# Kernel optimization log

Hardware: AMD Instinct MI355X
Metric: run time of the kernel (lower is better)

The kernel has to match this reference:

```python
import jax, jax.numpy as jnp
import numpy as np

B, S, D, H, E, K, DH = 4, 1024, 1024, 8, 4, 2, 128


def setup_inputs() -> dict:
    key = jax.random.key(0)
    ks = jax.random.split(key, 9)
    std = 1.0 / np.sqrt(D)
    f = lambda k, shape, s: jax.random.normal(k, shape, dtype=jnp.float32) * s
    return {
        'q_src': f(ks[0], (B, S, D), 1.0),
        'k_src': f(ks[1], (B, S, D), 1.0),
        'v_src': f(ks[2], (B, S, D), 1.0),
        'Wq': f(ks[3], (H * DH, D), std),
        'Wk': f(ks[4], (H * DH, D), std),
        'Wv': f(ks[5], (H * E, D, DH), std),
        'Wo': f(ks[6], (H * E, DH, D), 1.0 / np.sqrt(H * DH)),
        'sel_v': f(ks[7], (H * E, D), std),
        'sel_o': f(ks[8], (H * E, D), std),
    }


def _route(src, selw):
    # sigmoid-gated per-head top-k expert selection (get_sel), eval mode
    g = jax.nn.sigmoid((src @ selw.T).reshape(*src.shape[:-1], H, E))  # [B,S,H,E]
    val, idx = jax.lax.top_k(g, K)
    # dense per-expert mixture weights: zeros except top-k sigmoid gates
    return (jax.nn.one_hot(idx, E, dtype=g.dtype) * val[..., None]).sum(-2)  # [B,S,H,E]


def reference(q_src, k_src, v_src, Wq, Wk, Wv, Wo, sel_v, sel_o):
    scale = (1.0 / np.sqrt(DH)) ** 0.5  # scale.sqrt() applied to both q and k
    q = ((q_src @ Wq.T) * scale).reshape(B, S, H, DH).transpose(0, 2, 1, 3)  # [B,H,S,DH]
    k = ((k_src @ Wk.T) * scale).reshape(B, S, H, DH).transpose(0, 2, 1, 3)

    wv = _route(k_src, sel_v)  # [B,S,H,E] V-expert gates (from keys)
    wo = _route(q_src, sel_o)  # [B,S,H,E] O-expert gates (from queries)

    # cvmm V: per-token top-k mixture of expert V projections
    v_all = jnp.einsum('bsd,hedc->bshec', v_src, Wv.reshape(H, E, D, DH))
    v = jnp.einsum('bshec,bshe->bhsc', v_all, wv)  # [B,H,S,DH]

    att = jax.nn.softmax(jnp.einsum('bhqc,bhkc->bhqk', q, k), axis=-1)
    res = jnp.einsum('bhqk,bhkc->bqhc', att, v)  # [B,S,H,DH]

    # cvmm O: weight per-head outputs by gates, project and sum over heads/experts
    resw = res[..., None, :] * wo[..., None]  # [B,S,H,E,DH]
    out = jnp.einsum('bshec,hecd->bsd', resw, Wo.reshape(H, E, DH, D))
    return out
```

## Files before the change

kernel.cpp:

```cpp
#include <hip/hip_runtime.h>

#define DEV __device__ __forceinline__

typedef __attribute__((ext_vector_type(8))) short s8v;
typedef __attribute__((ext_vector_type(4))) short s4v;
typedef __attribute__((ext_vector_type(4))) float f4v;

DEV unsigned short f2b(float f){
    unsigned u = __float_as_uint(f);
    u = (u + 0x7FFFu + ((u >> 16) & 1u)) >> 16;
    return (unsigned short)u;
}
DEV float b2f(short s){ return __uint_as_float(((unsigned)(unsigned short)s) << 16); }

DEV unsigned cvtpk(float lo, float hi){
    unsigned r;
    asm("v_cvt_pk_bf16_f32 %0, %1, %2" : "=v"(r) : "v"(lo), "v"(hi));
    return r;
}
DEV float exp2v(float x){
    float r;
    asm("v_exp_f32 %0, %1" : "=v"(r) : "v"(x));
    return r;
}

DEV void gload16(const void* g, void* l){
    __builtin_amdgcn_global_load_lds(
        (const __attribute__((address_space(1))) unsigned*)g,
        (__attribute__((address_space(3))) unsigned*)l, 16, 0, 0);
}


DEV void stage2(const short* A, const short* B, int sA, int sB, int kA, int kB,
                short* la, short* lb, int w, int lane){
    int srow = lane >> 3;
    int swcol = ((lane & 7) ^ srow) << 3;
    #pragma unroll
    for(int it = 0; it < 4; it++){
        int seg = (w << 2) + it;
        int row = (seg << 3) + srow;
        gload16(&A[(size_t)row * sA + kA + swcol], &la[seg << 9]);
        gload16(&B[(size_t)row * sB + kB + swcol], &lb[seg << 9]);
    }
}

DEV void mfma_block(const short* la, const short* lb, int wm, int wn, int qr, int grp, f4v acc[4][4]){
    #pragma unroll
    for(int ks = 0; ks < 2; ks++){
        s8v af[4], bf[4];
        #pragma unroll
        for(int m = 0; m < 4; m++)
            af[m] = *(const s8v*)&la[(wm + m * 16 + qr) * 64 + ((((ks << 2) + grp) ^ (qr & 7)) << 3)];
        #pragma unroll
        for(int n = 0; n < 4; n++)
            bf[n] = *(const s8v*)&lb[(wn + n * 16 + qr) * 64 + ((((ks << 2) + grp) ^ (qr & 7)) << 3)];
        #pragma unroll
        for(int m = 0; m < 4; m++)
            #pragma unroll
            for(int n = 0; n < 4; n++)
                acc[m][n] = __builtin_amdgcn_mfma_f32_16x16x32_bf16(af[m], bf[n], acc[m][n], 0, 0, 0);
    }
}

__global__ __launch_bounds__(256) void k_cvt(const float* s0, const float* s1, const float* s2,
                                             const float* s3, const float* s4,
                                             short* o0, short* o1, short* o2, short* o3, short* o4){
    int y = blockIdx.y;
    const float* s = (y == 0) ? s0 : (y == 1) ? s1 : (y == 2) ? s2 : (y == 3) ? s3 : s4;
    short* o = (y == 0) ? o0 : (y == 1) ? o1 : (y == 2) ? o2 : (y == 3) ? o3 : o4;
    int n8 = (y < 3) ? 524288 : 131072;
    int idx = blockIdx.x * 256 + threadIdx.x;
    if(idx < n8){
        const float4* f = (const float4*)(s + (size_t)idx * 8);
        float4 a = f[0], b = f[1];
        s8v v;
        v[0] = f2b(a.x); v[1] = f2b(a.y); v[2] = f2b(a.z); v[3] = f2b(a.w);
        v[4] = f2b(b.x); v[5] = f2b(b.y); v[6] = f2b(b.z); v[7] = f2b(b.w);
        *(s8v*)(o + (size_t)idx * 8) = v;
    }
}

__global__ __launch_bounds__(256) void k_transpose(const float* in, short* out, int R, int C){
    in  += (size_t)blockIdx.z * R * C;
    out += (size_t)blockIdx.z * R * C;
    __shared__ float t[32][33];
    int c0 = blockIdx.x * 32, r0 = blockIdx.y * 32;
    int tx = threadIdx.x & 31, ty = threadIdx.x >> 5;
    #pragma unroll
    for(int p = 0; p < 4; p++){
        int r = p * 8 + ty;
        t[r][tx] = in[(size_t)(r0 + r) * C + c0 + tx];
    }
    __syncthreads();
    #pragma unroll
    for(int p = 0; p < 4; p++){
        int c = p * 8 + ty;
        out[(size_t)(c0 + c) * R + r0 + tx] = (short)f2b(t[tx][c]);
    }
}

__global__ __launch_bounds__(256) void k_rlogits(const float* qsrc, const float* ksrc,
                                                 const float* selv, const float* selo,
                                                 float* part){
    int which = blockIdx.y;
    const float* src = which ? qsrc : ksrc;
    const float* sel = which ? selo : selv;
    int tt = blockIdx.x >> 3, ks = blockIdx.x & 7;
    int tok0 = tt << 7;
    __shared__ float lsrc[128][36];
    __shared__ float lsel[32][36];
    int tid = threadIdx.x;
    int ts = tid & 31, es = tid >> 5;
    float acc[4][4];
    #pragma unroll
    for(int j = 0; j < 4; j++)
        #pragma unroll
        for(int i = 0; i < 4; i++) acc[j][i] = 0.f;

    #pragma unroll 1
    for(int c = 0; c < 4; c++){
        int k0 = (ks << 7) + (c << 5);
        {
            int row = tid >> 1, half = tid & 1;
            const float4* g = (const float4*)(src + (size_t)(tok0 + row) * 1024 + k0 + half * 16);
            #pragma unroll
            for(int qq = 0; qq < 4; qq++){
                int qw = half * 4 + qq;
                *(float4*)&lsrc[row][((qw + row) & 7) * 4] = g[qq];
            }
        }
        {
            int row = tid >> 3, qw = tid & 7;
            *(float4*)&lsel[row][((qw + row) & 7) * 4] =
                *(const float4*)(sel + (size_t)row * 1024 + k0 + qw * 4);
        }
        __syncthreads();
        #pragma unroll
        for(int q = 0; q < 8; q++){
            float4 sv[4];
            #pragma unroll
            for(int i = 0; i < 4; i++){
                int e = es * 4 + i;
                sv[i] = *(const float4*)&lsel[e][((q + e) & 7) * 4];
            }
            int slot = ((q + ts) & 7) * 4;
            #pragma unroll
            for(int j = 0; j < 4; j++){
                float4 xv = *(const float4*)&lsrc[ts + 32 * j][slot];
                #pragma unroll
                for(int i = 0; i < 4; i++){
                    acc[j][i] = fmaf(xv.x, sv[i].x, acc[j][i]);
                    acc[j][i] = fmaf(xv.y, sv[i].y, acc[j][i]);
                    acc[j][i] = fmaf(xv.z, sv[i].z, acc[j][i]);
                    acc[j][i] = fmaf(xv.w, sv[i].w, acc[j][i]);
                }
            }
        }
        __syncthreads();
    }
    #pragma unroll
    for(int j = 0; j < 4; j++){
        int token = tok0 + ts + 32 * j;
        f4v st;
        #pragma unroll
        for(int i = 0; i < 4; i++) st[i] = acc[j][i];
        *(f4v*)&part[(((size_t)(ks * 2 + which) * 4096) + token) * 32 + es * 4] = st;
    }
}

__global__ __launch_bounds__(256) void k_rfinal(const float* part, float* wvp, float* wop){
    int which = blockIdx.y;
    float* wout = which ? wop : wvp;
    int tid = threadIdx.x;
    int tok = blockIdx.x * 32 + (tid >> 3), h = tid & 7;
    f4v sum = {0.f, 0.f, 0.f, 0.f};
    #pragma unroll
    for(int s = 0; s < 8; s++)
        sum += *(const f4v*)&part[(((size_t)(s * 2 + which) * 4096) + tok) * 32 + h * 4];
    float g[4];
    #pragma unroll
    for(int e = 0; e < 4; e++) g[e] = 1.0f / (1.0f + expf(-sum[e]));
    f4v out;
    #pragma unroll
    for(int e = 0; e < 4; e++){
        int rank = 0;
        #pragma unroll
        for(int j = 0; j < 4; j++)
            rank += (g[j] > g[e]) || (g[j] == g[e] && j < e);
        out[e] = (rank < 2) ? g[e] : 0.0f;
    }
    *(f4v*)&wout[(size_t)tok * 32 + h * 4] = out;
}

__global__ __launch_bounds__(256) void k_count(const float* wv, int* cntv){
    int he = blockIdx.x, tid = threadIdx.x;
    __shared__ int red[256];
    int c = 0;
    #pragma unroll
    for(int p = 0; p < 16; p++)
        c += (wv[(size_t)(p * 256 + tid) * 32 + he] > 0.f) ? 1 : 0;
    red[tid] = c;
    __syncthreads();
    for(int s = 128; s > 0; s >>= 1){
        if(tid < s) red[tid] += red[tid + s];
        __syncthreads();
    }
    if(tid == 0) cntv[he] = red[0];
}

__global__ __launch_bounds__(256) void k_scan(const int* cntv, int* basev, int* descv){
    __shared__ int ntl[33];
    int tid = threadIdx.x;
    if(tid == 0){
        int run = 0;
        for(int he = 0; he < 32; he++){
            ntl[he] = run;
            run += (cntv[he] + 127) >> 7;
        }
        ntl[32] = run;
    }
    __syncthreads();
    if(tid < 32) basev[tid] = ntl[tid] << 7;
    for(int i = tid; i < 544; i += 256){
        int d = -1;
        for(int he = 0; he < 32; he++)
            if(i >= ntl[he] && i < ntl[he + 1]) d = he;
        descv[i] = d;
    }
}

__global__ __launch_bounds__(256) void k_gather(const float* wv, const int* basev,
                                                int* idxv, float* gbufv, int* rpos){
    int he = blockIdx.x, h = he >> 2, e = he & 3;
    int tid = threadIdx.x, lane = tid & 63, w = tid >> 6;
    int base = basev[he];
    __shared__ int wsum[4];
    __shared__ int running;
    if(tid == 0) running = 0;
    __syncthreads();
    #pragma unroll 1
    for(int p = 0; p < 16; p++){
        int t = p * 256 + tid;
        float g = wv[(size_t)t * 32 + he];
        bool sel = g > 0.f;
        unsigned long long m = __ballot(sel);
        int lpref = __popcll(m & ((1ull << lane) - 1ull));
        if(lane == 0) wsum[w] = __popcll(m);
        __syncthreads();
        int rb = running;
        int woff = 0;
        #pragma unroll
        for(int j = 0; j < 4; j++) woff += (j < w) ? wsum[j] : 0;
        if(sel){
            int pos = base + rb + woff + lpref;
            idxv[pos] = t;
            gbufv[pos] = g;
            int slot = 0;
            #pragma unroll
            for(int j = 0; j < 4; j++)
                slot += (j < e && wv[(size_t)t * 32 + h * 4 + j] > 0.f) ? 1 : 0;
            rpos[(size_t)t * 16 + h * 2 + slot] = pos;
        }
        __syncthreads();
        if(tid == 0) running += wsum[0] + wsum[1] + wsum[2] + wsum[3];
        __syncthreads();
    }
    int tot = running;
    int aligned = (tot + 127) & ~127;
    for(int i = tid; i < aligned - tot; i += 256){
        idxv[base + tot + i] = 0;
        gbufv[base + tot + i] = 0.f;
    }
}

__global__ __launch_bounds__(256) void k_gemmg(const short* vsb, const short* wvt,
                                               const int* descv, const int* idxv,
                                               const float* gbufv, short* Cg){
    int he = descv[blockIdx.x];
    if(he < 0) return;
    int row0 = (int)blockIdx.x << 7;
    __shared__ __align__(16) short la[2][8192];
    __shared__ __align__(16) short lb[2][8192];
    __shared__ int lidx[128];
    int tid = threadIdx.x, lane = tid & 63, w = tid >> 6;
    if(tid < 128) lidx[tid] = idxv[row0 + tid];
    __syncthreads();
    int srow = lane >> 3;
    int swcol = ((lane & 7) ^ srow) << 3;
    int arow[4];
    #pragma unroll
    for(int it = 0; it < 4; it++) arow[it] = lidx[(((w << 2) + it) << 3) + srow];
    const short* Bb = wvt + ((size_t)he << 17);
    int wm = (w >> 1) << 6, wn = (w & 1) << 6;
    int qr = lane & 15, grp = lane >> 4;
    f4v acc[4][4];
    #pragma unroll
    for(int m = 0; m < 4; m++)
        #pragma unroll
        for(int n = 0; n < 4; n++) acc[m][n] = f4v{0.f, 0.f, 0.f, 0.f};
    #pragma unroll 1
    for(int t = -1; t < 16; t++){
        int nxt = t + 1;
        if(nxt < 16){
            int buf = nxt & 1, k0 = nxt << 6;
            #pragma unroll
            for(int it = 0; it < 4; it++){
                int seg = (w << 2) + it;
                int row = (seg << 3) + srow;
                gload16(&vsb[(size_t)arow[it] * 1024 + k0 + swcol], &la[buf][seg << 9]);
                gload16(&Bb[(size_t)row * 1024 + k0 + swcol], &lb[buf][seg << 9]);
            }
        }
        if(t >= 0)
            mfma_block(la[t & 1], lb[t & 1], wm, wn, qr, grp, acc);
        __syncthreads();
    }
    #pragma unroll
    for(int m = 0; m < 4; m++){
        int rl = wm + m * 16 + (grp << 2);
        #pragma unroll
        for(int r = 0; r < 4; r++){
            float g = gbufv[row0 + rl + r];
            #pragma unroll
            for(int n = 0; n < 4; n++){
                int col = wn + n * 16 + qr;
                Cg[(size_t)(row0 + rl + r) * 128 + col] = (short)f2b(acc[m][n][r] * g);
            }
        }
    }
}

__global__ __launch_bounds__(256) void k_vcomb(const short* Cg, const int* rpos, short* vtg){
    int bh = blockIdx.y, b = bh >> 3, h = bh & 7;
    int s0 = blockIdx.x * 32;
    __shared__ __align__(16) short t0[32][136];
    __shared__ __align__(16) short t1[32][136];
    __shared__ int rl[32][2];
    int tid = threadIdx.x;
    if(tid < 64){
        int i = tid >> 1, s = tid & 1;
        rl[i][s] = rpos[(size_t)(b * 1024 + s0 + i) * 16 + h * 2 + s];
    }
    __syncthreads();
    #pragma unroll
    for(int p = 0; p < 4; p++){
        int ch = tid + p * 256;
        int i = ch >> 5, slot = (ch >> 4) & 1, c8 = (ch & 15) << 3;
        s8v v = *(const s8v*)&Cg[(size_t)rl[i][slot] * 128 + c8];
        if(slot) *(s8v*)&t1[i][c8] = v;
        else     *(s8v*)&t0[i][c8] = v;
    }
    __syncthreads();
    #pragma unroll
    for(int p = 0; p < 16; p++){
        int idx = tid + p * 256;
        int s = idx & 31, c = idx >> 5;
        float v = b2f(t0[s][c]) + b2f(t1[s][c]);
        vtg[((size_t)bh * 128 + c) * 1024 + s0 + s] = (short)f2b(v);
    }
}

__global__ __launch_bounds__(256) void k_gemmqk(const short* qsb, const short* ksb,
                                                const short* wqb, const short* wkb,
                                                short* qo, short* ko, float scale){
    __shared__ __align__(16) short la[2][8192];
    __shared__ __align__(16) short lb[2][8192];
    int wg = (blockIdx.x & 7) * 64 + (blockIdx.x >> 3);
    int which = wg >> 8, tl = wg & 255;
    int mt = tl >> 3, nt = tl & 7;
    const short* A = (which ? ksb : qsb) + ((size_t)(mt << 7)) * 1024;
    const short* B = (which ? wkb : wqb) + ((size_t)(nt << 7)) * 1024;
    short* out = which ? ko : qo;
    int tid = threadIdx.x, lane = tid & 63, w = tid >> 6;
    int wm = (w >> 1) << 6, wn = (w & 1) << 6;
    int qr = lane & 15, grp = lane >> 4;
    f4v acc[4][4];
    #pragma unroll
    for(int m = 0; m < 4; m++)
        #pragma unroll
        for(int n = 0; n < 4; n++) acc[m][n] = f4v{0.f, 0.f, 0.f, 0.f};
    #pragma unroll 1
    for(int t = -1; t < 16; t++){
        int nxt = t + 1;
        if(nxt < 16)
            stage2(A, B, 1024, 1024, nxt << 6, nxt << 6, la[nxt & 1], lb[nxt & 1], w, lane);
        if(t >= 0)
            mfma_block(la[t & 1], lb[t & 1], wm, wn, qr, grp, acc);
        __syncthreads();
    }
    #pragma unroll
    for(int m = 0; m < 4; m++){
        int rb = (mt << 7) + wm + m * 16 + (grp << 2);
        #pragma unroll
        for(int n = 0; n < 4; n++){
            int col = (nt << 7) + wn + n * 16 + qr;
            #pragma unroll
            for(int r = 0; r < 4; r++)
                out[(size_t)(rb + r) * 1024 + col] = (short)f2b(acc[m][n][r] * scale);
        }
    }
}

__global__ __launch_bounds__(256) void k_gemmo(const short* resw, const short* wot, float* po){
    __shared__ __align__(16) short la[2][8192];
    __shared__ __align__(16) short lb[2][8192];
    int wg = (blockIdx.x & 7) * 64 + (blockIdx.x >> 3);
    int ksp = wg & 1, tile = wg >> 1;
    int mt = tile >> 3, nt = tile & 7;
    const short* A = resw + (size_t)(mt << 7) * 4096 + ksp * 2048;
    const short* B = wot + (size_t)(nt << 7) * 4096 + ksp * 2048;
    int tid = threadIdx.x, lane = tid & 63, w = tid >> 6;
    int wm = (w >> 1) << 6, wn = (w & 1) << 6;
    int qr = lane & 15, grp = lane >> 4;
    f4v acc[4][4];
    #pragma unroll
    for(int m = 0; m < 4; m++)
        #pragma unroll
        for(int n = 0; n < 4; n++) acc[m][n] = f4v{0.f, 0.f, 0.f, 0.f};
    #pragma unroll 1
    for(int t = -1; t < 32; t++){
        int nxt = t + 1;
        if(nxt < 32)
            stage2(A, B, 4096, 4096, nxt << 6, nxt << 6, la[nxt & 1], lb[nxt & 1], w, lane);
        if(t >= 0)
            mfma_block(la[t & 1], lb[t & 1], wm, wn, qr, grp, acc);
        __syncthreads();
    }
    po += (size_t)ksp * 4194304;
    #pragma unroll
    for(int m = 0; m < 4; m++){
        int rb = (mt << 7) + wm + m * 16 + (grp << 2);
        #pragma unroll
        for(int n = 0; n < 4; n++){
            int col = (nt << 7) + wn + n * 16 + qr;
            #pragma unroll
            for(int r = 0; r < 4; r++)
                po[(size_t)(rb + r) * 1024 + col] = acc[m][n][r];
        }
    }
}

__global__ __launch_bounds__(256) void k_red(const float* p0, const float* p1, float* out){
    size_t idx = ((size_t)blockIdx.x * 256 + threadIdx.x) * 4;
    f4v a = *(const f4v*)&p0[idx];
    f4v b = *(const f4v*)&p1[idx];
    f4v s = a + b;
    *(f4v*)&out[idx] = s;
}

__global__ __launch_bounds__(256) void k_attn(const short* qg, const short* kg,
                                              const short* vtg, const float* wo, short* resw){
    __shared__ __align__(16) short lk[2][8192];
    __shared__ __align__(16) short lv[2][8192];
    __shared__ __align__(16) short pl[4][16 * 72];
    int bh = blockIdx.y, b = bh >> 3, h = bh & 7;
    int w = threadIdx.x >> 6, lane = threadIdx.x & 63;
    int qr = lane & 15, grp = lane >> 4;
    int q0 = blockIdx.x * 64 + w * 16;
    const short* vtb = vtg + ((size_t)bh << 17);
    short* pw = &pl[w][0];

    int tok = b * 1024 + q0 + qr;
    s8v qf[4];
    #pragma unroll
    for(int ks = 0; ks < 4; ks++)
        qf[ks] = *(const s8v*)&qg[(size_t)tok * 1024 + h * 128 + ks * 32 + grp * 8];
    f4v o[8];
    #pragma unroll
    for(int ct = 0; ct < 8; ct++) o[ct] = f4v{0.f, 0.f, 0.f, 0.f};
    float m_cur = -1e30f, l_cur = 0.f;

    int klr = lane >> 4, klc = lane & 15;
    int vlr = lane >> 3, vlc = lane & 7;

    #pragma unroll 1
    for(int t = -1; t < 16; t++){
        int nxt = t + 1;
        if(nxt < 16){
            int buf = nxt & 1, kv0 = nxt << 6;
            #pragma unroll
            for(int i = 0; i < 4; i++){
                int seg = (w << 2) + i;
                int kr = (seg << 2) + klr;
                int kc = klc ^ (kr & 7);
                gload16(&kg[(size_t)(b * 1024 + kv0 + kr) * 1024 + h * 128 + kc * 8], &lk[buf][seg << 9]);
                int vr = (seg << 3) + vlr;
                int vc = vlc ^ (vr & 7);
                gload16(&vtb[(size_t)vr * 1024 + kv0 + vc * 8], &lv[buf][seg << 9]);
            }
        }
        if(t >= 0){
            int cur = t & 1;
            f4v s[4];
            #pragma unroll
            for(int kt = 0; kt < 4; kt++) s[kt] = f4v{0.f, 0.f, 0.f, 0.f};
            __builtin_amdgcn_s_setprio(1);
            #pragma unroll
            for(int ks = 0; ks < 4; ks++){
                #pragma unroll
                for(int kt = 0; kt < 4; kt++){
                    int row = kt * 16 + qr;
                    s8v kf = *(const s8v*)&lk[cur][row * 128 + ((((ks << 2) + grp) ^ (row & 7)) << 3)];
                    s[kt] = __builtin_amdgcn_mfma_f32_16x16x32_bf16(kf, qf[ks], s[kt], 0, 0, 0);
                }
            }
            __builtin_amdgcn_s_setprio(0);
            float pm = s[0][0];
            #pragma unroll
            for(int kt = 0; kt < 4; kt++)
                #pragma unroll
                for(int r = 0; r < 4; r++) pm = fmaxf(pm, s[kt][r]);
            pm = fmaxf(pm, __shfl_xor(pm, 16));
            pm = fmaxf(pm, __shfl_xor(pm, 32));
            if(!__all(pm - m_cur <= 11.541f)){
                float mn = fmaxf(m_cur, pm);
                float fs = exp2v(m_cur - mn);
                #pragma unroll
                for(int ct = 0; ct < 8; ct++){
                    o[ct][0] *= fs; o[ct][1] *= fs; o[ct][2] *= fs; o[ct][3] *= fs;
                }
                l_cur *= fs;
                m_cur = mn;
            }
            float ps = 0.f;
            #pragma unroll
            for(int kt = 0; kt < 4; kt++)
                #pragma unroll
                for(int r = 0; r < 4; r++){
                    s[kt][r] = exp2v(s[kt][r] - m_cur);
                    ps += s[kt][r];
                }
            ps += __shfl_xor(ps, 16);
            ps += __shfl_xor(ps, 32);
            l_cur += ps;
            #pragma unroll
            for(int kt = 0; kt < 4; kt++){
                uint2 pv;
                pv.x = cvtpk(s[kt][0], s[kt][1]);
                pv.y = cvtpk(s[kt][2], s[kt][3]);
                *(uint2*)&pw[qr * 72 + kt * 16 + grp * 4] = pv;
            }
            s8v pf0 = *(const s8v*)&pw[qr * 72 + grp * 8];
            s8v pf1 = *(const s8v*)&pw[qr * 72 + 32 + grp * 8];
            __builtin_amdgcn_s_setprio(1);
            #pragma unroll
            for(int ct = 0; ct < 8; ct++){
                int row = ct * 16 + qr;
                s8v vf0 = *(const s8v*)&lv[cur][row * 64 + ((grp ^ (row & 7)) << 3)];
                s8v vf1 = *(const s8v*)&lv[cur][row * 64 + (((4 + grp) ^ (row & 7)) << 3)];
                o[ct] = __builtin_amdgcn_mfma_f32_16x16x32_bf16(vf0, pf0, o[ct], 0, 0, 0);
                o[ct] = __builtin_amdgcn_mfma_f32_16x16x32_bf16(vf1, pf1, o[ct], 0, 0, 0);
            }
            __builtin_amdgcn_s_setprio(0);
        }
        __syncthreads();
    }
    float inv = 1.0f / l_cur;
    float g4[4];
    #pragma unroll
    for(int e = 0; e < 4; e++) g4[e] = wo[(size_t)tok * 32 + h * 4 + e];
    #pragma unroll
    for(int ct = 0; ct < 8; ct++){
        float v0 = o[ct][0] * inv, v1 = o[ct][1] * inv;
        float v2 = o[ct][2] * inv, v3 = o[ct][3] * inv;
        #pragma unroll
        for(int e = 0; e < 4; e++){
            uint2 sv;
            sv.x = cvtpk(v0 * g4[e], v1 * g4[e]);
            sv.y = cvtpk(v2 * g4[e], v3 * g4[e]);
            *(uint2*)&resw[(size_t)tok * 4096 + (h * 4 + e) * 128 + ct * 16 + grp * 4] = sv;
        }
    }
}

extern "C" void kernel_launch(void* const* d_in, const int* in_sizes, int n_in,
                              void* d_out, int out_size, void* d_ws, size_t ws_size,
                              hipStream_t stream){
    const float* q_src = (const float*)d_in[0];
    const float* k_src = (const float*)d_in[1];
    const float* v_src = (const float*)d_in[2];
    const float* Wq    = (const float*)d_in[3];
    const float* Wk    = (const float*)d_in[4];
    const float* Wv    = (const float*)d_in[5];
    const float* Wo    = (const float*)d_in[6];
    const float* selv  = (const float*)d_in[7];
    const float* selo  = (const float*)d_in[8];

    const size_t MB = 1ull << 20;
    char* ws = (char*)d_ws;
    short* qsb  = (short*)(ws + 0 * MB);
    short* ksb  = (short*)(ws + 8 * MB);
    short* vsb  = (short*)(ws + 16 * MB);
    short* wqb  = (short*)(ws + 24 * MB);
    short* wkb  = (short*)(ws + 26 * MB);
    short* wvt  = (short*)(ws + 28 * MB);
    short* wot  = (short*)(ws + 36 * MB);
    short* q    = (short*)(ws + 44 * MB);
    short* k    = (short*)(ws + 52 * MB);
    short* vt   = (short*)(ws + 60 * MB);
    float* wv   = (float*)(ws + 76 * MB);
    float* wo   = (float*)(ws + 76 * MB + 524288);
    float* part = (float*)(ws + 80 * MB);
    short* Cg   = (short*)(ws + 80 * MB);
    int*   cntv = (int*)  (ws + 100 * MB);
    int*   basev= (int*)  (ws + 100 * MB + 4096);
    int*   descv= (int*)  (ws + 100 * MB + 8192);
    int*   idxv = (int*)  (ws + 101 * MB);
    float* gbufv= (float*)(ws + 102 * MB);
    int*   rposv= (int*)  (ws + 103 * MB);
    short* resw = (short*)(ws + 0 * MB);
    float* po   = (float*)(ws + 80 * MB);

    const float qk_scale = 0.29730177875068026f * 1.2011224087864498f;

    k_cvt<<<dim3(2048, 5), 256, 0, stream>>>(q_src, k_src, v_src, Wq, Wk, qsb, ksb, vsb, wqb, wkb);
    k_transpose<<<dim3(4, 32, 32), 256, 0, stream>>>(Wv, wvt, 1024, 128);
    k_transpose<<<dim3(32, 128, 1), 256, 0, stream>>>(Wo, wot, 4096, 1024);
    k_rlogits<<<dim3(256, 2), 256, 0, stream>>>(q_src, k_src, selv, selo, part);
    k_rfinal<<<dim3(128, 2), 256, 0, stream>>>(part, wv, wo);
    k_count<<<dim3(32), 256, 0, stream>>>(wv, cntv);
    k_scan<<<dim3(1), 256, 0, stream>>>(cntv, basev, descv);
    k_gather<<<dim3(32), 256, 0, stream>>>(wv, basev, idxv, gbufv, rposv);
    k_gemmqk<<<dim3(512), 256, 0, stream>>>(qsb, ksb, wqb, wkb, q, k, qk_scale);
    k_gemmg<<<dim3(544), 256, 0, stream>>>(vsb, wvt, descv, idxv, gbufv, Cg);
    k_vcomb<<<dim3(32, 32), 256, 0, stream>>>(Cg, rposv, vt);
    k_attn<<<dim3(16, 32), 256, 0, stream>>>(q, k, vt, wo, resw);
    k_gemmo<<<dim3(512), 256, 0, stream>>>(resw, wot, po);
    k_red<<<dim3(4096), 256, 0, stream>>>(po, po + 4194304, (float*)d_out);
}
```

Baseline: 225.7 us.

## Replace split-K reduction with atomics and shrink attention blocks to two waves

The output GEMM now accumulates its two split-K halves directly into the zeroed output with float atomics. This removes the partial buffer writes and the separate reduction kernel, at the cost of an extra zeroing kernel and atomic traffic. The attention kernel now uses 128-thread blocks covering 32 queries, launched as twice as many blocks. It drops the double-buffered K/V prefetch in favour of single-buffered loads with barriers, which raises block count and occupancy but loses load/compute overlap.

```diff
diff --git a/kernel.cpp b/kernel.cpp
--- a/kernel.cpp
+++ b/kernel.cpp
@@ -60,6 +60,11 @@
             for(int n = 0; n < 4; n++)
                 acc[m][n] = __builtin_amdgcn_mfma_f32_16x16x32_bf16(af[m], bf[n], acc[m][n], 0, 0, 0);
     }
+}
+
+__global__ __launch_bounds__(256) void k_zero(float* out){
+    size_t idx = ((size_t)blockIdx.x * 256 + threadIdx.x) * 4;
+    *(f4v*)&out[idx] = f4v{0.f, 0.f, 0.f, 0.f};
 }
 
 __global__ __launch_bounds__(256) void k_cvt(const float* s0, const float* s1, const float* s2,
@@ -401,7 +406,7 @@
     }
 }
 
-__global__ __launch_bounds__(256) void k_gemmo(const short* resw, const short* wot, float* po){
+__global__ __launch_bounds__(256) void k_gemmo(const short* resw, const short* wot, float* out){
     __shared__ __align__(16) short la[2][8192];
     __shared__ __align__(16) short lb[2][8192];
     int wg = (blockIdx.x & 7) * 64 + (blockIdx.x >> 3);
@@ -426,7 +431,6 @@
             mfma_block(la[t & 1], lb[t & 1], wm, wn, qr, grp, acc);
         __syncthreads();
     }
-    po += (size_t)ksp * 4194304;
     #pragma unroll
     for(int m = 0; m < 4; m++){
         int rb = (mt << 7) + wm + m * 16 + (grp << 2);
@@ -435,28 +439,20 @@
             int col = (nt << 7) + wn + n * 16 + qr;
             #pragma unroll
             for(int r = 0; r < 4; r++)
-                po[(size_t)(rb + r) * 1024 + col] = acc[m][n][r];
-        }
-    }
-}
-
-__global__ __launch_bounds__(256) void k_red(const float* p0, const float* p1, float* out){
-    size_t idx = ((size_t)blockIdx.x * 256 + threadIdx.x) * 4;
-    f4v a = *(const f4v*)&p0[idx];
-    f4v b = *(const f4v*)&p1[idx];
-    f4v s = a + b;
-    *(f4v*)&out[idx] = s;
-}
-
-__global__ __launch_bounds__(256) void k_attn(const short* qg, const short* kg,
+                unsafeAtomicAdd(&out[(size_t)(rb + r) * 1024 + col], acc[m][n][r]);
+        }
+    }
+}
+
+__global__ __launch_bounds__(128) void k_attn(const short* qg, const short* kg,
                                               const short* vtg, const float* wo, short* resw){
-    __shared__ __align__(16) short lk[2][8192];
-    __shared__ __align__(16) short lv[2][8192];
-    __shared__ __align__(16) short pl[4][16 * 72];
+    __shared__ __align__(16) short lk[8192];
+    __shared__ __align__(16) short lv[8192];
+    __shared__ __align__(16) short pl[2][16 * 72];
     int bh = blockIdx.y, b = bh >> 3, h = bh & 7;
     int w = threadIdx.x >> 6, lane = threadIdx.x & 63;
     int qr = lane & 15, grp = lane >> 4;
-    int q0 = blockIdx.x * 64 + w * 16;
+    int q0 = blockIdx.x * 32 + w * 16;
     const short* vtb = vtg + ((size_t)bh << 17);
     short* pw = &pl[w][0];
 
@@ -474,86 +470,81 @@
     int vlr = lane >> 3, vlc = lane & 7;
 
     #pragma unroll 1
-    for(int t = -1; t < 16; t++){
-        int nxt = t + 1;
-        if(nxt < 16){
-            int buf = nxt & 1, kv0 = nxt << 6;
-            #pragma unroll
-            for(int i = 0; i < 4; i++){
-                int seg = (w << 2) + i;
-                int kr = (seg << 2) + klr;
-                int kc = klc ^ (kr & 7);
-                gload16(&kg[(size_t)(b * 1024 + kv0 + kr) * 1024 + h * 128 + kc * 8], &lk[buf][seg << 9]);
-                int vr = (seg << 3) + vlr;
-                int vc = vlc ^ (vr & 7);
-                gload16(&vtb[(size_t)vr * 1024 + kv0 + vc * 8], &lv[buf][seg << 9]);
-            }
-        }
-        if(t >= 0){
-            int cur = t & 1;
-            f4v s[4];
-            #pragma unroll
-            for(int kt = 0; kt < 4; kt++) s[kt] = f4v{0.f, 0.f, 0.f, 0.f};
-            __builtin_amdgcn_s_setprio(1);
-            #pragma unroll
-            for(int ks = 0; ks < 4; ks++){
-                #pragma unroll
-                for(int kt = 0; kt < 4; kt++){
-                    int row = kt * 16 + qr;
-                    s8v kf = *(const s8v*)&lk[cur][row * 128 + ((((ks << 2) + grp) ^ (row & 7)) << 3)];
-                    s[kt] = __builtin_amdgcn_mfma_f32_16x16x32_bf16(kf, qf[ks], s[kt], 0, 0, 0);
-                }
-            }
-            __builtin_amdgcn_s_setprio(0);
-            float pm = s[0][0];
-            #pragma unroll
-            for(int kt = 0; kt < 4; kt++)
-                #pragma unroll
-                for(int r = 0; r < 4; r++) pm = fmaxf(pm, s[kt][r]);
-            pm = fmaxf(pm, __shfl_xor(pm, 16));
-            pm = fmaxf(pm, __shfl_xor(pm, 32));
-            if(!__all(pm - m_cur <= 11.541f)){
-                float mn = fmaxf(m_cur, pm);
-                float fs = exp2v(m_cur - mn);
-                #pragma unroll
-                for(int ct = 0; ct < 8; ct++){
-                    o[ct][0] *= fs; o[ct][1] *= fs; o[ct][2] *= fs; o[ct][3] *= fs;
-                }
-                l_cur *= fs;
-                m_cur = mn;
-            }
-            float ps = 0.f;
-            #pragma unroll
-            for(int kt = 0; kt < 4; kt++)
-                #pragma unroll
-                for(int r = 0; r < 4; r++){
-                    s[kt][r] = exp2v(s[kt][r] - m_cur);
-                    ps += s[kt][r];
-                }
-            ps += __shfl_xor(ps, 16);
-            ps += __shfl_xor(ps, 32);
-            l_cur += ps;
+    for(int t = 0; t < 16; t++){
+        int kv0 = t << 6;
+        if(t) __syncthreads();
+        #pragma unroll
+        for(int i = 0; i < 8; i++){
+            int seg = w * 8 + i;
+            int kr = (seg << 2) + klr;
+            int kc = klc ^ (kr & 7);
+            gload16(&kg[(size_t)(b * 1024 + kv0 + kr) * 1024 + h * 128 + kc * 8], &lk[seg << 9]);
+            int vr = (seg << 3) + vlr;
+            int vc = vlc ^ (vr & 7);
+            gload16(&vtb[(size_t)vr * 1024 + kv0 + vc * 8], &lv[seg << 9]);
+        }
+        __syncthreads();
+        f4v s[4];
+        #pragma unroll
+        for(int kt = 0; kt < 4; kt++) s[kt] = f4v{0.f, 0.f, 0.f, 0.f};
+        __builtin_amdgcn_s_setprio(1);
+        #pragma unroll
+        for(int ks = 0; ks < 4; ks++){
             #pragma unroll
             for(int kt = 0; kt < 4; kt++){
-                uint2 pv;
-                pv.x = cvtpk(s[kt][0], s[kt][1]);
-                pv.y = cvtpk(s[kt][2], s[kt][3]);
-                *(uint2*)&pw[qr * 72 + kt * 16 + grp * 4] = pv;
-            }
-            s8v pf0 = *(const s8v*)&pw[qr * 72 + grp * 8];
-            s8v pf1 = *(const s8v*)&pw[qr * 72 + 32 + grp * 8];
-            __builtin_amdgcn_s_setprio(1);
+                int row = kt * 16 + qr;
+                s8v kf = *(const s8v*)&lk[row * 128 + ((((ks << 2) + grp) ^ (row & 7)) << 3)];
+                s[kt] = __builtin_amdgcn_mfma_f32_16x16x32_bf16(kf, qf[ks], s[kt], 0, 0, 0);
+            }
+        }
+        __builtin_amdgcn_s_setprio(0);
+        float pm = s[0][0];
+        #pragma unroll
+        for(int kt = 0; kt < 4; kt++)
+            #pragma unroll
+            for(int r = 0; r < 4; r++) pm = fmaxf(pm, s[kt][r]);
+        pm = fmaxf(pm, __shfl_xor(pm, 16));
+        pm = fmaxf(pm, __shfl_xor(pm, 32));
+        if(!__all(pm - m_cur <= 11.541f)){
+            float mn = fmaxf(m_cur, pm);
+            float fs = exp2v(m_cur - mn);
             #pragma unroll
             for(int ct = 0; ct < 8; ct++){
-                int row = ct * 16 + qr;
-                s8v vf0 = *(const s8v*)&lv[cur][row * 64 + ((grp ^ (row & 7)) << 3)];
-                s8v vf1 = *(const s8v*)&lv[cur][row * 64 + (((4 + grp) ^ (row & 7)) << 3)];
-                o[ct] = __builtin_amdgcn_mfma_f32_16x16x32_bf16(vf0, pf0, o[ct], 0, 0, 0);
-                o[ct] = __builtin_amdgcn_mfma_f32_16x16x32_bf16(vf1, pf1, o[ct], 0, 0, 0);
-            }
-            __builtin_amdgcn_s_setprio(0);
-        }
-        __syncthreads();
+                o[ct][0] *= fs; o[ct][1] *= fs; o[ct][2] *= fs; o[ct][3] *= fs;
+            }
+            l_cur *= fs;
+            m_cur = mn;
+        }
+        float ps = 0.f;
+        #pragma unroll
+        for(int kt = 0; kt < 4; kt++)
+            #pragma unroll
+            for(int r = 0; r < 4; r++){
+                s[kt][r] = exp2v(s[kt][r] - m_cur);
+                ps += s[kt][r];
+            }
+        ps += __shfl_xor(ps, 16);
+        ps += __shfl_xor(ps, 32);
+        l_cur += ps;
+        #pragma unroll
+        for(int kt = 0; kt < 4; kt++){
+            uint2 pv;
+            pv.x = cvtpk(s[kt][0], s[kt][1]);
+            pv.y = cvtpk(s[kt][2], s[kt][3]);
+            *(uint2*)&pw[qr * 72 + kt * 16 + grp * 4] = pv;
+        }
+        s8v pf0 = *(const s8v*)&pw[qr * 72 + grp * 8];
+        s8v pf1 = *(const s8v*)&pw[qr * 72 + 32 + grp * 8];
+        __builtin_amdgcn_s_setprio(1);
+        #pragma unroll
+        for(int ct = 0; ct < 8; ct++){
+            int row = ct * 16 + qr;
+            s8v vf0 = *(const s8v*)&lv[row * 64 + ((grp ^ (row & 7)) << 3)];
+            s8v vf1 = *(const s8v*)&lv[row * 64 + (((4 + grp) ^ (row & 7)) << 3)];
+            o[ct] = __builtin_amdgcn_mfma_f32_16x16x32_bf16(vf0, pf0, o[ct], 0, 0, 0);
+            o[ct] = __builtin_amdgcn_mfma_f32_16x16x32_bf16(vf1, pf1, o[ct], 0, 0, 0);
+        }
+        __builtin_amdgcn_s_setprio(0);
     }
     float inv = 1.0f / l_cur;
     float g4[4];
@@ -609,10 +600,10 @@
     float* gbufv= (float*)(ws + 102 * MB);
     int*   rposv= (int*)  (ws + 103 * MB);
     short* resw = (short*)(ws + 0 * MB);
-    float* po   = (float*)(ws + 80 * MB);
 
     const float qk_scale = 0.29730177875068026f * 1.2011224087864498f;
 
+    k_zero<<<dim3(4096), 256, 0, stream>>>((float*)d_out);
     k_cvt<<<dim3(2048, 5), 256, 0, stream>>>(q_src, k_src, v_src, Wq, Wk, qsb, ksb, vsb, wqb, wkb);
     k_transpose<<<dim3(4, 32, 32), 256, 0, stream>>>(Wv, wvt, 1024, 128);
     k_transpose<<<dim3(32, 128, 1), 256, 0, stream>>>(Wo, wot, 4096, 1024);
@@ -624,7 +615,6 @@
     k_gemmqk<<<dim3(512), 256, 0, stream>>>(qsb, ksb, wqb, wkb, q, k, qk_scale);
     k_gemmg<<<dim3(544), 256, 0, stream>>>(vsb, wvt, descv, idxv, gbufv, Cg);
     k_vcomb<<<dim3(32, 32), 256, 0, stream>>>(Cg, rposv, vt);
-    k_attn<<<dim3(16, 32), 256, 0, stream>>>(q, k, vt, wo, resw);
-    k_gemmo<<<dim3(512), 256, 0, stream>>>(resw, wot, po);
-    k_red<<<dim3(4096), 256, 0, stream>>>(po, po + 4194304, (float*)d_out);
-}
+    k_attn<<<dim3(32, 32), 128, 0, stream>>>(q, k, vt, wo, resw);
+    k_gemmo<<<dim3(512), 256, 0, stream>>>(resw, wot, (float*)d_out);
+}
```

Result: slower. 246.8 us (+9.4%).
